# Kernel tuning notes

Measured on AMD Instinct MI355X. Metric: run time of the kernel, lower is better.

## Reference

```python
import jax, jax.numpy as jnp
import numpy as np

D_MODEL = 2048
N_HEADS = 16
HEAD_DIM = D_MODEL // N_HEADS
ROPE_THETA = 10000.0
B, S = 2, 2048
MAX_POS = 8192


def _rope(x, position_ids):
    # x: [b, h, s, hd]; position_ids: [b, s] int
    half = HEAD_DIM // 2
    inv_freq = 1.0 / (ROPE_THETA ** (jnp.arange(0, HEAD_DIM, 2, dtype=jnp.float32) / HEAD_DIM))  # [half]
    ang = position_ids[..., None].astype(jnp.float32) * inv_freq  # [b, s, half]
    cos = jnp.concatenate([jnp.cos(ang), jnp.cos(ang)], axis=-1)[:, None]  # [b, 1, s, hd]
    sin = jnp.concatenate([jnp.sin(ang), jnp.sin(ang)], axis=-1)[:, None]
    x1, x2 = x[..., :half], x[..., half:]
    rot = jnp.concatenate([-x2, x1], axis=-1)  # rotate_half
    return x * cos + rot * sin


def setup_inputs() -> dict:
    key = jax.random.key(0)
    ks = jax.random.split(key, 6)
    wscale = 1.0 / np.sqrt(D_MODEL)
    x_sparse = jax.random.normal(ks[0], (B, S, D_MODEL), dtype=jnp.float32)
    Wq = jax.random.normal(ks[1], (D_MODEL, D_MODEL), dtype=jnp.float32) * wscale
    Wk = jax.random.normal(ks[2], (D_MODEL, D_MODEL), dtype=jnp.float32) * wscale
    Wv = jax.random.normal(ks[3], (D_MODEL, D_MODEL), dtype=jnp.float32) * wscale
    Wo = jax.random.normal(ks[4], (D_MODEL, D_MODEL), dtype=jnp.float32) * wscale
    position_ids = jnp.sort(jax.random.randint(ks[5], (B, S), 0, MAX_POS), axis=-1).astype(jnp.int64)
    return {"x_sparse": x_sparse, "Wq": Wq, "Wk": Wk, "Wv": Wv, "Wo": Wo, "position_ids": position_ids}


def reference(x_sparse, Wq, Wk, Wv, Wo, position_ids):
    b, s, d = x_sparse.shape

    def heads(W):
        return (x_sparse @ W).reshape(b, s, N_HEADS, HEAD_DIM).transpose(0, 2, 1, 3)  # [b,h,s,hd]

    q = _rope(heads(Wq), position_ids)
    k = _rope(heads(Wk), position_ids)
    v = heads(Wv)

    scores = jnp.einsum('bhqd,bhkd->bhqk', q, k) / np.float32(np.sqrt(HEAD_DIM))
    # dynamic position-based causal mask: pos_i >= pos_j, broadcast over heads
    mask = position_ids[:, None, :, None] >= position_ids[:, None, None, :]  # [b,1,s,s]
    scores = jnp.where(mask, scores, jnp.float32(-1e30))
    attn = jax.nn.softmax(scores, axis=-1)
    out = jnp.einsum('bhqk,bhkd->bhqd', attn, v)  # [b,h,s,hd]
    out = out.transpose(0, 2, 1, 3).reshape(b, s, d)
    return out @ Wo
```

## Files before the change

kernel.cpp:

```cpp
#include <hip/hip_runtime.h>
#include <stdint.h>


typedef unsigned short u16;
typedef unsigned int u32;
typedef __attribute__((ext_vector_type(8))) short bf16x8;
typedef __attribute__((ext_vector_type(4))) float f32x4;

#define SEQ 2048
#define DM 2048
#define NH 16
#define HD 128
#define SM_SCALE 0.08838834764831845f
#define K2LOG 0.12751743f

__device__ __forceinline__ u16 f2bf(float f) {
  union { float f; uint32_t u; } v; v.f = f;
  uint32_t u = v.u + 0x7fffu + ((v.u >> 16) & 1u);
  return (u16)(u >> 16);
}
__device__ __forceinline__ float bf2f(u16 h) {
  union { uint32_t u; float f; } v; v.u = ((uint32_t)h) << 16; return v.f;
}
__device__ __forceinline__ u32 pack2(float a, float b) {
  return (u32)f2bf(a) | ((u32)f2bf(b) << 16);
}
__device__ __forceinline__ u32 pack2_trunc(float a, float b) {
  union { float f; u32 u; } x, y; x.f = a; y.f = b;
  return (x.u >> 16) | (y.u & 0xFFFF0000u);
}

__device__ __forceinline__ void gl2lds16(const void* g, void* l) {
  __builtin_amdgcn_global_load_lds(
      (const __attribute__((address_space(1))) uint32_t*)g,
      (__attribute__((address_space(3))) uint32_t*)l, 16, 0, 0);
}

__global__ __launch_bounds__(256) void cvt_x(const float* __restrict__ x, u16* __restrict__ xb) {
  int i = blockIdx.x * 256 + threadIdx.x;
  float4 v = ((const float4*)x)[i];
  uint2 r;
  r.x = pack2(v.x, v.y);
  r.y = pack2(v.z, v.w);
  ((uint2*)xb)[i] = r;
}

__global__ __launch_bounds__(256) void wtrans(const float* __restrict__ w0, const float* __restrict__ w1,
                                              const float* __restrict__ w2, const float* __restrict__ w3,
                                              u16* __restrict__ dst) {
  const float* W = blockIdx.z == 0 ? w0 : blockIdx.z == 1 ? w1 : blockIdx.z == 2 ? w2 : w3;
  u16* D = dst + (size_t)blockIdx.z * DM * DM;
  int k0 = blockIdx.x * 32, n0 = blockIdx.y * 32;
  __shared__ u16 t[32][33];
  int tx = threadIdx.x, ty = threadIdx.y;
#pragma unroll
  for (int i = 0; i < 32; i += 8)
    t[ty + i][tx] = f2bf(W[(size_t)(k0 + ty + i) * DM + n0 + tx]);
  __syncthreads();
#pragma unroll
  for (int i = 0; i < 32; i += 8)
    D[(size_t)(n0 + ty + i) * DM + k0 + tx] = t[tx][ty + i];
}

__device__ __forceinline__ void gemm_core(const u16* __restrict__ A, const u16* __restrict__ Bt,
                                          int m0, int n0, u16* As, u16* Bs, f32x4 acc[4][4]) {
  int tid = threadIdx.x, lane = tid & 63;
  int l15 = lane & 15, quad = lane >> 4;
  int wave = tid >> 6;
  int wm = (wave >> 1) * 64, wn = (wave & 1) * 64;
  for (int k0 = 0; k0 < DM; k0 += 64) {
#pragma unroll
    for (int i = 0; i < 4; ++i) {
      int s = i * 256 + tid;
      int row = s >> 3, c = (s & 7) ^ (row & 7);
      gl2lds16(&A[(size_t)(m0 + row) * DM + k0 + c * 8], &As[(s & ~63) * 8]);
      gl2lds16(&Bt[(size_t)(n0 + row) * DM + k0 + c * 8], &Bs[(s & ~63) * 8]);
    }
    __syncthreads();
#pragma unroll
    for (int kk = 0; kk < 2; ++kk) {
      bf16x8 af[4], bfr[4];
#pragma unroll
      for (int mt = 0; mt < 4; ++mt) {
        int row = wm + mt * 16 + l15;
        int c = (kk * 4 + quad) ^ (row & 7);
        af[mt] = *(const bf16x8*)&As[row * 64 + c * 8];
      }
#pragma unroll
      for (int nt = 0; nt < 4; ++nt) {
        int row = wn + nt * 16 + l15;
        int c = (kk * 4 + quad) ^ (row & 7);
        bfr[nt] = *(const bf16x8*)&Bs[row * 64 + c * 8];
      }
#pragma unroll
      for (int mt = 0; mt < 4; ++mt)
#pragma unroll
        for (int nt = 0; nt < 4; ++nt)
          acc[mt][nt] = __builtin_amdgcn_mfma_f32_16x16x32_bf16(af[mt], bfr[nt], acc[mt][nt], 0, 0, 0);
    }
    __syncthreads();
  }
}

__global__ __launch_bounds__(256) void qkv_gemm(const u16* __restrict__ X, const u16* __restrict__ Wt,
                                                u16* __restrict__ Qo, u16* __restrict__ Ko,
                                                u16* __restrict__ Vto) {
  __shared__ u16 As[128 * 64];
  __shared__ u16 Bs[128 * 64];
  const u16* Bt = Wt + (size_t)blockIdx.z * DM * DM;
  int n0 = blockIdx.x * 128, m0 = blockIdx.y * 128;
  f32x4 acc[4][4] = {};
  gemm_core(X, Bt, m0, n0, As, Bs, acc);
  int lane = threadIdx.x & 63, wave = threadIdx.x >> 6;
  int l15 = lane & 15, quad = lane >> 4;
  int wm = (wave >> 1) * 64, wn = (wave & 1) * 64;
  if (blockIdx.z == 2) {
    int h = n0 >> 7;
#pragma unroll
    for (int mt = 0; mt < 4; ++mt)
#pragma unroll
      for (int nt = 0; nt < 4; ++nt) {
        int tok = m0 + wm + mt * 16 + quad * 4;
        int d = wn + nt * 16 + l15;
        int b = tok >> 11, sx = tok & (SEQ - 1);
        u16* dp = &Vto[((size_t)(b * NH + h) * HD + d) * SEQ + sx];
        *(u32*)&dp[0] = pack2(acc[mt][nt][0], acc[mt][nt][1]);
        *(u32*)&dp[2] = pack2(acc[mt][nt][2], acc[mt][nt][3]);
      }
  } else {
    u16* C = blockIdx.z == 0 ? Qo : Ko;
#pragma unroll
    for (int mt = 0; mt < 4; ++mt)
#pragma unroll
      for (int nt = 0; nt < 4; ++nt)
#pragma unroll
        for (int r = 0; r < 4; ++r)
          C[(size_t)(m0 + wm + mt * 16 + quad * 4 + r) * DM + n0 + wn + nt * 16 + l15]
              = f2bf(acc[mt][nt][r]);
  }
}

__global__ __launch_bounds__(256) void proj_gemm(const u16* __restrict__ A, const u16* __restrict__ Wt,
                                                 float* __restrict__ C) {
  __shared__ u16 As[128 * 64];
  __shared__ u16 Bs[128 * 64];
  int n0 = blockIdx.x * 128, m0 = blockIdx.y * 128;
  f32x4 acc[4][4] = {};
  gemm_core(A, Wt, m0, n0, As, Bs, acc);
  int lane = threadIdx.x & 63, wave = threadIdx.x >> 6;
  int l15 = lane & 15, quad = lane >> 4;
  int wm = (wave >> 1) * 64, wn = (wave & 1) * 64;
#pragma unroll
  for (int mt = 0; mt < 4; ++mt)
#pragma unroll
    for (int nt = 0; nt < 4; ++nt)
#pragma unroll
      for (int r = 0; r < 4; ++r)
        C[(size_t)(m0 + wm + mt * 16 + quad * 4 + r) * DM + n0 + wn + nt * 16 + l15] = acc[mt][nt][r];
}

__global__ __launch_bounds__(256) void rope_k(u16* __restrict__ Q, u16* __restrict__ K,
                                              const int* __restrict__ pos) {
  uint32_t idx = blockIdx.x * 256 + threadIdx.x;
  int i = idx & 63;
  int h = (idx >> 6) & 15;
  int s = (idx >> 10) & 2047;
  int b = idx >> 21;
  u16* P = (blockIdx.y == 0) ? Q : K;
  int p = pos[b * SEQ + s];
  float inv_rev = exp2f(fmaf((float)i, -0.20762051f, -2.6514961f));
  float pf = (float)p;
  float hi = pf * inv_rev;
  float err = fmaf(pf, inv_rev, -hi);
  float r = (hi - truncf(hi)) + err;
  float ang = r * 6.2831853f;
  float sn = __sinf(ang), cs = __cosf(ang);
  size_t base = ((size_t)(b * SEQ + s)) * DM + h * HD;
  float x1 = bf2f(P[base + i]), x2 = bf2f(P[base + 64 + i]);
  P[base + i] = f2bf(x1 * cs - x2 * sn);
  P[base + 64 + i] = f2bf(x2 * cs + x1 * sn);
}

__global__ __launch_bounds__(256, 2) void attn_k(const u16* __restrict__ Q, const u16* __restrict__ K,
                                                 const u16* __restrict__ Vt, const int* __restrict__ pos,
                                                 u16* __restrict__ AO) {
  int tid = threadIdx.x, lane = tid & 63, wave = tid >> 6;
  int J = blockIdx.x * 4 + wave;
  int bh = J & 31;
  int t = J >> 5;
  int stripe = (t < 32) ? (2 * t) : (127 - 2 * t);
  int b = bh >> 4, h = bh & 15;
  int l15 = lane & 15, quad = lane >> 4;
  const int* posb = pos + b * SEQ;
  int qbase = stripe * 32;
  const u16* Kbase = &K[(size_t)(b * SEQ) * DM + h * HD];
  const u16* Vbase = &Vt[(size_t)(b * NH + h) * HD * SEQ];

  bf16x8 qf[2][4];
#pragma unroll
  for (int qi = 0; qi < 2; ++qi)
#pragma unroll
    for (int kk = 0; kk < 4; ++kk)
      qf[qi][kk] = *(const bf16x8*)&Q[(size_t)(b * SEQ + qbase + qi * 16 + l15) * DM
                                      + h * HD + kk * 32 + quad * 8];

  auto ub = [&](int v) {
    int c = 0;
#pragma unroll
    for (int st = 1024; st; st >>= 1)
      if (posb[c + st - 1] <= v) c += st;
    if (c == 2047 && posb[2047] <= v) c = 2048;
    return c;
  };
  int cnt[2];
  cnt[0] = ub(posb[qbase + l15]);
  cnt[1] = ub(posb[qbase + 16 + l15]);
  int cnt_min = ub(posb[qbase]);
  int cnt_max = ub(posb[qbase + 31]);
  int ntile = (cnt_max + 63) >> 6;

  float m_i[2] = {-1.0e30f, -1.0e30f}, l_i[2] = {0.0f, 0.0f};
  f32x4 oacc[2][8] = {};

  int base0 = l15 + ((quad & 1) << 5);
  bool hi_sel = (quad >> 1) != 0;

  for (int j = 0; j < ntile; ++j) {
    int j0 = j * 64;
    bf16x8 kf[4][4];
#pragma unroll
    for (int kk = 0; kk < 4; ++kk)
#pragma unroll
      for (int kt = 0; kt < 4; ++kt)
        kf[kk][kt] = *(const bf16x8*)&Kbase[(size_t)(j0 + kt * 16 + l15) * DM + kk * 32 + quad * 8];

    f32x4 sacc[2][4] = {};
#pragma unroll
    for (int kk = 0; kk < 4; ++kk)
#pragma unroll
      for (int qi = 0; qi < 2; ++qi)
#pragma unroll
        for (int kt = 0; kt < 4; ++kt)
          sacc[qi][kt] = __builtin_amdgcn_mfma_f32_16x16x32_bf16(kf[kk][kt], qf[qi][kk], sacc[qi][kt], 0, 0, 0);

    bf16x8 vf[2][8];
#pragma unroll
    for (int kk2 = 0; kk2 < 2; ++kk2)
#pragma unroll
      for (int dt = 0; dt < 8; ++dt)
        vf[kk2][dt] = *(const bf16x8*)&Vbase[(size_t)(dt * 16 + l15) * SEQ + j0 + kk2 * 32 + quad * 8];

    bool need_mask = (j0 + 64 > cnt_min);
    u32 pb[2][4][2];
#pragma unroll
    for (int qi = 0; qi < 2; ++qi) {
      if (need_mask) {
        int rel = cnt[qi] - j0;
#pragma unroll
        for (int kt = 0; kt < 4; ++kt)
#pragma unroll
          for (int r = 0; r < 4; ++r)
            if (kt * 16 + quad * 4 + r >= rel) sacc[qi][kt][r] = -1.0e30f;
      }
      float mx = fmaxf(fmaxf(sacc[qi][0][0], sacc[qi][0][1]), fmaxf(sacc[qi][0][2], sacc[qi][0][3]));
#pragma unroll
      for (int kt = 1; kt < 4; ++kt)
        mx = fmaxf(mx, fmaxf(fmaxf(sacc[qi][kt][0], sacc[qi][kt][1]),
                             fmaxf(sacc[qi][kt][2], sacc[qi][kt][3])));
      mx = fmaxf(mx, __shfl_xor(mx, 16));
      mx = fmaxf(mx, __shfl_xor(mx, 32));
      float mold = m_i[qi];
      float mn = fmaxf(mold, mx);
      if (__any(mn > mold)) {
        float al = exp2f((mold - mn) * K2LOG);
        l_i[qi] *= al;
#pragma unroll
        for (int dt = 0; dt < 8; ++dt) oacc[qi][dt] *= al;
        m_i[qi] = mn;
      }
      float nc = -m_i[qi] * K2LOG;
      float rs = 0.0f;
#pragma unroll
      for (int kt = 0; kt < 4; ++kt) {
        float p0 = exp2f(fmaf(sacc[qi][kt][0], K2LOG, nc));
        float p1 = exp2f(fmaf(sacc[qi][kt][1], K2LOG, nc));
        float p2 = exp2f(fmaf(sacc[qi][kt][2], K2LOG, nc));
        float p3 = exp2f(fmaf(sacc[qi][kt][3], K2LOG, nc));
        rs += (p0 + p1) + (p2 + p3);
        pb[qi][kt][0] = pack2_trunc(p0, p1);
        pb[qi][kt][1] = pack2_trunc(p2, p3);
      }
      rs += __shfl_xor(rs, 16);
      rs += __shfl_xor(rs, 32);
      l_i[qi] += rs;
    }

#pragma unroll
    for (int kk2 = 0; kk2 < 2; ++kk2) {
#pragma unroll
      for (int qi = 0; qi < 2; ++qi) {
        u32 w[4];
#pragma unroll
        for (int wd = 0; wd < 4; ++wd) {
          int src = base0 + ((wd >> 1) << 4);
          u32 va = __shfl(pb[qi][kk2 * 2 + 0][wd & 1], src);
          u32 vb = __shfl(pb[qi][kk2 * 2 + 1][wd & 1], src);
          w[wd] = hi_sel ? vb : va;
        }
        union { bf16x8 v; u32 u[4]; } pt;
        pt.u[0] = w[0]; pt.u[1] = w[1]; pt.u[2] = w[2]; pt.u[3] = w[3];
#pragma unroll
        for (int dt = 0; dt < 8; ++dt)
          oacc[qi][dt] = __builtin_amdgcn_mfma_f32_16x16x32_bf16(vf[kk2][dt], pt.v, oacc[qi][dt], 0, 0, 0);
      }
    }
  }

#pragma unroll
  for (int qi = 0; qi < 2; ++qi) {
    float inv = 1.0f / l_i[qi];
    u16* aop = &AO[(size_t)(b * SEQ + qbase + qi * 16 + l15) * DM + h * HD];
#pragma unroll
    for (int dt = 0; dt < 8; ++dt) {
      int col = dt * 16 + quad * 4;
      *(u32*)&aop[col]     = pack2(oacc[qi][dt][0] * inv, oacc[qi][dt][1] * inv);
      *(u32*)&aop[col + 2] = pack2(oacc[qi][dt][2] * inv, oacc[qi][dt][3] * inv);
    }
  }
}

extern "C" void kernel_launch(void* const* d_in, const int* in_sizes, int n_in,
                              void* d_out, int out_size, void* d_ws, size_t ws_size,
                              hipStream_t stream) {
  const float* x  = (const float*)d_in[0];
  const float* Wq = (const float*)d_in[1];
  const float* Wk = (const float*)d_in[2];
  const float* Wv = (const float*)d_in[3];
  const float* Wo = (const float*)d_in[4];
  const int*  pos = (const int*)d_in[5];
  float* out = (float*)d_out;

  u16* ws  = (u16*)d_ws;
  u16* xb  = ws;
  u16* wt  = xb  + (size_t)4096 * 2048;
  u16* qb  = wt  + (size_t)4 * 2048 * 2048;
  u16* kb  = qb  + (size_t)4096 * 2048;
  u16* vtb = kb  + (size_t)4096 * 2048;
  u16* aob = vtb + (size_t)4096 * 2048;

  cvt_x<<<8192, 256, 0, stream>>>(x, xb);
  wtrans<<<dim3(64, 64, 4), dim3(32, 8), 0, stream>>>(Wq, Wk, Wv, Wo, wt);
  qkv_gemm<<<dim3(16, 32, 3), 256, 0, stream>>>(xb, wt, qb, kb, vtb);
  rope_k<<<dim3(16384, 2), 256, 0, stream>>>(qb, kb, pos);
  attn_k<<<dim3(512), 256, 0, stream>>>(qb, kb, vtb, pos, aob);
  proj_gemm<<<dim3(16, 32), 256, 0, stream>>>(aob, wt + (size_t)3 * 2048 * 2048, out);
}
```

Before: 451.5 us.

## Split attention KV tiles across wave pairs and merge partial softmax via LDS

Each 32-row query stripe is now handled by two waves that process alternating 64-key tiles, and their partial max, sum and output accumulators are combined through shared memory at the end. The grid doubles and launch bounds rise to four blocks per CU. The aim is more parallelism and better latency hiding on the long causal stripes of the attention kernel. The cost is about 36KB of LDS per block, a block-wide barrier plus a merge step, and added register pressure from the higher occupancy target, which may cause spills.

Result: slower. 848.4 us (+87.9%).

```diff
diff --git a/kernel.cpp b/kernel.cpp
--- a/kernel.cpp
+++ b/kernel.cpp
@@ -181,11 +181,16 @@
   P[base + 64 + i] = f2bf(x2 * cs + x1 * sn);
 }
 
-__global__ __launch_bounds__(256, 2) void attn_k(const u16* __restrict__ Q, const u16* __restrict__ K,
+__global__ __launch_bounds__(256, 4) void attn_k(const u16* __restrict__ Q, const u16* __restrict__ K,
                                                  const u16* __restrict__ Vt, const int* __restrict__ pos,
                                                  u16* __restrict__ AO) {
+  __shared__ f32x4 ldsO[2][2][8][64];
+  __shared__ float ldsM[2][2][64];
+  __shared__ float ldsL[2][2][64];
   int tid = threadIdx.x, lane = tid & 63, wave = tid >> 6;
-  int J = blockIdx.x * 4 + wave;
+  int pair = wave >> 1;
+  int half = wave & 1;
+  int J = blockIdx.x * 2 + pair;
   int bh = J & 31;
   int t = J >> 5;
   int stripe = (t < 32) ? (2 * t) : (127 - 2 * t);
@@ -225,7 +230,7 @@
   int base0 = l15 + ((quad & 1) << 5);
   bool hi_sel = (quad >> 1) != 0;
 
-  for (int j = 0; j < ntile; ++j) {
+  for (int j = half; j < ntile; j += 2) {
     int j0 = j * 64;
     bf16x8 kf[4][4];
 #pragma unroll
@@ -316,15 +321,35 @@
     }
   }
 
-#pragma unroll
-  for (int qi = 0; qi < 2; ++qi) {
-    float inv = 1.0f / l_i[qi];
-    u16* aop = &AO[(size_t)(b * SEQ + qbase + qi * 16 + l15) * DM + h * HD];
-#pragma unroll
-    for (int dt = 0; dt < 8; ++dt) {
-      int col = dt * 16 + quad * 4;
-      *(u32*)&aop[col]     = pack2(oacc[qi][dt][0] * inv, oacc[qi][dt][1] * inv);
-      *(u32*)&aop[col + 2] = pack2(oacc[qi][dt][2] * inv, oacc[qi][dt][3] * inv);
+  if (half) {
+#pragma unroll
+    for (int qi = 0; qi < 2; ++qi) {
+      ldsM[pair][qi][lane] = m_i[qi];
+      ldsL[pair][qi][lane] = l_i[qi];
+#pragma unroll
+      for (int dt = 0; dt < 8; ++dt) ldsO[pair][qi][dt][lane] = oacc[qi][dt];
+    }
+  }
+  __syncthreads();
+  if (!half) {
+#pragma unroll
+    for (int qi = 0; qi < 2; ++qi) {
+      float mB = ldsM[pair][qi][lane];
+      float lB = ldsL[pair][qi][lane];
+      float mN = fmaxf(m_i[qi], mB);
+      float aA = exp2f((m_i[qi] - mN) * K2LOG);
+      float aB = exp2f((mB - mN) * K2LOG);
+      float inv = 1.0f / fmaf(l_i[qi], aA, lB * aB);
+      float sA = aA * inv, sB = aB * inv;
+      u16* aop = &AO[(size_t)(b * SEQ + qbase + qi * 16 + l15) * DM + h * HD];
+#pragma unroll
+      for (int dt = 0; dt < 8; ++dt) {
+        f32x4 ob = ldsO[pair][qi][dt][lane];
+        f32x4 oa = oacc[qi][dt];
+        int col = dt * 16 + quad * 4;
+        *(u32*)&aop[col]     = pack2(fmaf(oa[0], sA, ob[0] * sB), fmaf(oa[1], sA, ob[1] * sB));
+        *(u32*)&aop[col + 2] = pack2(fmaf(oa[2], sA, ob[2] * sB), fmaf(oa[3], sA, ob[3] * sB));
+      }
     }
   }
 }
@@ -352,6 +377,6 @@
   wtrans<<<dim3(64, 64, 4), dim3(32, 8), 0, stream>>>(Wq, Wk, Wv, Wo, wt);
   qkv_gemm<<<dim3(16, 32, 3), 256, 0, stream>>>(xb, wt, qb, kb, vtb);
   rope_k<<<dim3(16384, 2), 256, 0, stream>>>(qb, kb, pos);
-  attn_k<<<dim3(512), 256, 0, stream>>>(qb, kb, vtb, pos, aob);
+  attn_k<<<dim3(1024), 256, 0, stream>>>(qb, kb, vtb, pos, aob);
   proj_gemm<<<dim3(16, 32), 256, 0, stream>>>(aob, wt + (size_t)3 * 2048 * 2048, out);
 }
```

## Shrink attention per-wave query tile to 16 rows for higher occupancy

Applied to the files above, without the earlier changes.

Each wave in the attention kernel now handles 16 query rows instead of 32, and the grid doubles to 1024 blocks. Launch bounds rise to 4 blocks per CU, and K/V fragments are loaded per inner step rather than all at once, which cuts register pressure. The aim is more resident waves to hide global-load latency. In exchange, each K/V tile loaded from global memory is reused across half as many query rows, so total K/V traffic roughly doubles.

Result: slower. 576.1 us (+27.6%).

```diff
diff --git a/kernel.cpp b/kernel.cpp
--- a/kernel.cpp
+++ b/kernel.cpp
@@ -181,28 +181,26 @@
   P[base + 64 + i] = f2bf(x2 * cs + x1 * sn);
 }
 
-__global__ __launch_bounds__(256, 2) void attn_k(const u16* __restrict__ Q, const u16* __restrict__ K,
+__global__ __launch_bounds__(256, 4) void attn_k(const u16* __restrict__ Q, const u16* __restrict__ K,
                                                  const u16* __restrict__ Vt, const int* __restrict__ pos,
                                                  u16* __restrict__ AO) {
   int tid = threadIdx.x, lane = tid & 63, wave = tid >> 6;
   int J = blockIdx.x * 4 + wave;
   int bh = J & 31;
   int t = J >> 5;
-  int stripe = (t < 32) ? (2 * t) : (127 - 2 * t);
+  int stripe = (t < 64) ? (2 * t) : (255 - 2 * t);
   int b = bh >> 4, h = bh & 15;
   int l15 = lane & 15, quad = lane >> 4;
   const int* posb = pos + b * SEQ;
-  int qbase = stripe * 32;
+  int qbase = stripe * 16;
   const u16* Kbase = &K[(size_t)(b * SEQ) * DM + h * HD];
   const u16* Vbase = &Vt[(size_t)(b * NH + h) * HD * SEQ];
 
-  bf16x8 qf[2][4];
-#pragma unroll
-  for (int qi = 0; qi < 2; ++qi)
-#pragma unroll
-    for (int kk = 0; kk < 4; ++kk)
-      qf[qi][kk] = *(const bf16x8*)&Q[(size_t)(b * SEQ + qbase + qi * 16 + l15) * DM
-                                      + h * HD + kk * 32 + quad * 8];
+  bf16x8 qf[4];
+#pragma unroll
+  for (int kk = 0; kk < 4; ++kk)
+    qf[kk] = *(const bf16x8*)&Q[(size_t)(b * SEQ + qbase + l15) * DM
+                                + h * HD + kk * 32 + quad * 8];
 
   auto ub = [&](int v) {
     int c = 0;
@@ -212,120 +210,105 @@
     if (c == 2047 && posb[2047] <= v) c = 2048;
     return c;
   };
-  int cnt[2];
-  cnt[0] = ub(posb[qbase + l15]);
-  cnt[1] = ub(posb[qbase + 16 + l15]);
+  int cnt = ub(posb[qbase + l15]);
   int cnt_min = ub(posb[qbase]);
-  int cnt_max = ub(posb[qbase + 31]);
+  int cnt_max = ub(posb[qbase + 15]);
   int ntile = (cnt_max + 63) >> 6;
 
-  float m_i[2] = {-1.0e30f, -1.0e30f}, l_i[2] = {0.0f, 0.0f};
-  f32x4 oacc[2][8] = {};
+  float m_i = -1.0e30f, l_i = 0.0f;
+  f32x4 oacc[8] = {};
 
   int base0 = l15 + ((quad & 1) << 5);
   bool hi_sel = (quad >> 1) != 0;
 
   for (int j = 0; j < ntile; ++j) {
     int j0 = j * 64;
-    bf16x8 kf[4][4];
-#pragma unroll
-    for (int kk = 0; kk < 4; ++kk)
-#pragma unroll
-      for (int kt = 0; kt < 4; ++kt)
-        kf[kk][kt] = *(const bf16x8*)&Kbase[(size_t)(j0 + kt * 16 + l15) * DM + kk * 32 + quad * 8];
-
-    f32x4 sacc[2][4] = {};
-#pragma unroll
-    for (int kk = 0; kk < 4; ++kk)
-#pragma unroll
-      for (int qi = 0; qi < 2; ++qi)
+
+    f32x4 sacc[4] = {};
+#pragma unroll
+    for (int kt = 0; kt < 4; ++kt) {
+      bf16x8 kfa[4];
+#pragma unroll
+      for (int kk = 0; kk < 4; ++kk)
+        kfa[kk] = *(const bf16x8*)&Kbase[(size_t)(j0 + kt * 16 + l15) * DM + kk * 32 + quad * 8];
+#pragma unroll
+      for (int kk = 0; kk < 4; ++kk)
+        sacc[kt] = __builtin_amdgcn_mfma_f32_16x16x32_bf16(kfa[kk], qf[kk], sacc[kt], 0, 0, 0);
+    }
+
+    bool need_mask = (j0 + 64 > cnt_min);
+    u32 pb[4][2];
+    {
+      if (need_mask) {
+        int rel = cnt - j0;
 #pragma unroll
         for (int kt = 0; kt < 4; ++kt)
-          sacc[qi][kt] = __builtin_amdgcn_mfma_f32_16x16x32_bf16(kf[kk][kt], qf[qi][kk], sacc[qi][kt], 0, 0, 0);
-
-    bf16x8 vf[2][8];
-#pragma unroll
-    for (int kk2 = 0; kk2 < 2; ++kk2)
-#pragma unroll
-      for (int dt = 0; dt < 8; ++dt)
-        vf[kk2][dt] = *(const bf16x8*)&Vbase[(size_t)(dt * 16 + l15) * SEQ + j0 + kk2 * 32 + quad * 8];
-
-    bool need_mask = (j0 + 64 > cnt_min);
-    u32 pb[2][4][2];
-#pragma unroll
-    for (int qi = 0; qi < 2; ++qi) {
-      if (need_mask) {
-        int rel = cnt[qi] - j0;
-#pragma unroll
-        for (int kt = 0; kt < 4; ++kt)
 #pragma unroll
           for (int r = 0; r < 4; ++r)
-            if (kt * 16 + quad * 4 + r >= rel) sacc[qi][kt][r] = -1.0e30f;
-      }
-      float mx = fmaxf(fmaxf(sacc[qi][0][0], sacc[qi][0][1]), fmaxf(sacc[qi][0][2], sacc[qi][0][3]));
+            if (kt * 16 + quad * 4 + r >= rel) sacc[kt][r] = -1.0e30f;
+      }
+      float mx = fmaxf(fmaxf(sacc[0][0], sacc[0][1]), fmaxf(sacc[0][2], sacc[0][3]));
 #pragma unroll
       for (int kt = 1; kt < 4; ++kt)
-        mx = fmaxf(mx, fmaxf(fmaxf(sacc[qi][kt][0], sacc[qi][kt][1]),
-                             fmaxf(sacc[qi][kt][2], sacc[qi][kt][3])));
+        mx = fmaxf(mx, fmaxf(fmaxf(sacc[kt][0], sacc[kt][1]),
+                             fmaxf(sacc[kt][2], sacc[kt][3])));
       mx = fmaxf(mx, __shfl_xor(mx, 16));
       mx = fmaxf(mx, __shfl_xor(mx, 32));
-      float mold = m_i[qi];
+      float mold = m_i;
       float mn = fmaxf(mold, mx);
       if (__any(mn > mold)) {
         float al = exp2f((mold - mn) * K2LOG);
-        l_i[qi] *= al;
-#pragma unroll
-        for (int dt = 0; dt < 8; ++dt) oacc[qi][dt] *= al;
-        m_i[qi] = mn;
-      }
-      float nc = -m_i[qi] * K2LOG;
+        l_i *= al;
+#pragma unroll
+        for (int dt = 0; dt < 8; ++dt) oacc[dt] *= al;
+        m_i = mn;
+      }
+      float nc = -m_i * K2LOG;
       float rs = 0.0f;
 #pragma unroll
       for (int kt = 0; kt < 4; ++kt) {
-        float p0 = exp2f(fmaf(sacc[qi][kt][0], K2LOG, nc));
-        float p1 = exp2f(fmaf(sacc[qi][kt][1], K2LOG, nc));
-        float p2 = exp2f(fmaf(sacc[qi][kt][2], K2LOG, nc));
-        float p3 = exp2f(fmaf(sacc[qi][kt][3], K2LOG, nc));
+        float p0 = exp2f(fmaf(sacc[kt][0], K2LOG, nc));
+        float p1 = exp2f(fmaf(sacc[kt][1], K2LOG, nc));
+        float p2 = exp2f(fmaf(sacc[kt][2], K2LOG, nc));
+        float p3 = exp2f(fmaf(sacc[kt][3], K2LOG, nc));
         rs += (p0 + p1) + (p2 + p3);
-        pb[qi][kt][0] = pack2_trunc(p0, p1);
-        pb[qi][kt][1] = pack2_trunc(p2, p3);
+        pb[kt][0] = pack2_trunc(p0, p1);
+        pb[kt][1] = pack2_trunc(p2, p3);
       }
       rs += __shfl_xor(rs, 16);
       rs += __shfl_xor(rs, 32);
-      l_i[qi] += rs;
+      l_i += rs;
     }
 
 #pragma unroll
     for (int kk2 = 0; kk2 < 2; ++kk2) {
-#pragma unroll
-      for (int qi = 0; qi < 2; ++qi) {
-        u32 w[4];
-#pragma unroll
-        for (int wd = 0; wd < 4; ++wd) {
-          int src = base0 + ((wd >> 1) << 4);
-          u32 va = __shfl(pb[qi][kk2 * 2 + 0][wd & 1], src);
-          u32 vb = __shfl(pb[qi][kk2 * 2 + 1][wd & 1], src);
-          w[wd] = hi_sel ? vb : va;
-        }
-        union { bf16x8 v; u32 u[4]; } pt;
-        pt.u[0] = w[0]; pt.u[1] = w[1]; pt.u[2] = w[2]; pt.u[3] = w[3];
-#pragma unroll
-        for (int dt = 0; dt < 8; ++dt)
-          oacc[qi][dt] = __builtin_amdgcn_mfma_f32_16x16x32_bf16(vf[kk2][dt], pt.v, oacc[qi][dt], 0, 0, 0);
-      }
+      bf16x8 vf[8];
+#pragma unroll
+      for (int dt = 0; dt < 8; ++dt)
+        vf[dt] = *(const bf16x8*)&Vbase[(size_t)(dt * 16 + l15) * SEQ + j0 + kk2 * 32 + quad * 8];
+      u32 w[4];
+#pragma unroll
+      for (int wd = 0; wd < 4; ++wd) {
+        int src = base0 + ((wd >> 1) << 4);
+        u32 va = __shfl(pb[kk2 * 2 + 0][wd & 1], src);
+        u32 vb = __shfl(pb[kk2 * 2 + 1][wd & 1], src);
+        w[wd] = hi_sel ? vb : va;
+      }
+      union { bf16x8 v; u32 u[4]; } pt;
+      pt.u[0] = w[0]; pt.u[1] = w[1]; pt.u[2] = w[2]; pt.u[3] = w[3];
+#pragma unroll
+      for (int dt = 0; dt < 8; ++dt)
+        oacc[dt] = __builtin_amdgcn_mfma_f32_16x16x32_bf16(vf[dt], pt.v, oacc[dt], 0, 0, 0);
     }
   }
 
-#pragma unroll
-  for (int qi = 0; qi < 2; ++qi) {
-    float inv = 1.0f / l_i[qi];
-    u16* aop = &AO[(size_t)(b * SEQ + qbase + qi * 16 + l15) * DM + h * HD];
-#pragma unroll
-    for (int dt = 0; dt < 8; ++dt) {
-      int col = dt * 16 + quad * 4;
-      *(u32*)&aop[col]     = pack2(oacc[qi][dt][0] * inv, oacc[qi][dt][1] * inv);
-      *(u32*)&aop[col + 2] = pack2(oacc[qi][dt][2] * inv, oacc[qi][dt][3] * inv);
-    }
+  float inv = 1.0f / l_i;
+  u16* aop = &AO[(size_t)(b * SEQ + qbase + l15) * DM + h * HD];
+#pragma unroll
+  for (int dt = 0; dt < 8; ++dt) {
+    int col = dt * 16 + quad * 4;
+    *(u32*)&aop[col]     = pack2(oacc[dt][0] * inv, oacc[dt][1] * inv);
+    *(u32*)&aop[col + 2] = pack2(oacc[dt][2] * inv, oacc[dt][3] * inv);
   }
 }
 
@@ -352,6 +335,6 @@
   wtrans<<<dim3(64, 64, 4), dim3(32, 8), 0, stream>>>(Wq, Wk, Wv, Wo, wt);
   qkv_gemm<<<dim3(16, 32, 3), 256, 0, stream>>>(xb, wt, qb, kb, vtb);
   rope_k<<<dim3(16384, 2), 256, 0, stream>>>(qb, kb, pos);
-  attn_k<<<dim3(512), 256, 0, stream>>>(qb, kb, vtb, pos, aob);
+  attn_k<<<dim3(1024), 256, 0, stream>>>(qb, kb, vtb, pos, aob);
   proj_gemm<<<dim3(16, 32), 256, 0, stream>>>(aob, wt + (size_t)3 * 2048 * 2048, out);
 }
```

## Share K/V tiles across waves via double-buffered LDS staging in attention

Applied to the files above, without the earlier changes.

Each block now handles four adjacent query stripes of the same batch-head instead of four independent stripes. K and V tiles are staged once per block into swizzled, double-buffered LDS with async global-to-LDS copies, replacing the per-wave direct global loads. The block-level tile count follows the last stripe, and waves with fewer tiles idle through the barriers. This cuts redundant global/L2 traffic at the cost of 64KB of LDS, per-tile __syncthreads, and load imbalance between waves.

Result: faster. 425.5 us (-5.8%).

```diff
diff --git a/kernel.cpp b/kernel.cpp
--- a/kernel.cpp
+++ b/kernel.cpp
@@ -184,17 +184,20 @@
 __global__ __launch_bounds__(256, 2) void attn_k(const u16* __restrict__ Q, const u16* __restrict__ K,
                                                  const u16* __restrict__ Vt, const int* __restrict__ pos,
                                                  u16* __restrict__ AO) {
+  __shared__ u16 Ks[2][64 * 128];
+  __shared__ u16 Vs[2][128 * 64];
   int tid = threadIdx.x, lane = tid & 63, wave = tid >> 6;
-  int J = blockIdx.x * 4 + wave;
-  int bh = J & 31;
-  int t = J >> 5;
-  int stripe = (t < 32) ? (2 * t) : (127 - 2 * t);
+  int bx = blockIdx.x;
+  int bh = bx & 31;
+  int g4 = bx >> 5;
+  int g = (bh & 1) ? (15 - g4) : g4;
   int b = bh >> 4, h = bh & 15;
+  int stripe = 4 * g + wave;
   int l15 = lane & 15, quad = lane >> 4;
   const int* posb = pos + b * SEQ;
   int qbase = stripe * 32;
-  const u16* Kbase = &K[(size_t)(b * SEQ) * DM + h * HD];
-  const u16* Vbase = &Vt[(size_t)(b * NH + h) * HD * SEQ];
+  const u16* Kg = &K[(size_t)(b * SEQ) * DM + h * HD];
+  const u16* Vg = &Vt[(size_t)(b * NH + h) * HD * SEQ];
 
   bf16x8 qf[2][4];
 #pragma unroll
@@ -218,6 +221,22 @@
   int cnt_min = ub(posb[qbase]);
   int cnt_max = ub(posb[qbase + 31]);
   int ntile = (cnt_max + 63) >> 6;
+  int cnt_blk = ub(posb[(4 * g + 3) * 32 + 31]);
+  int ntile_blk = (cnt_blk + 63) >> 6;
+
+  auto STAGE = [&](int j0, int bufi) {
+#pragma unroll
+    for (int i = 0; i < 4; ++i) {
+      int s = i * 256 + tid;
+      int rk = s >> 4, ck = (s & 15) ^ (rk & 15);
+      gl2lds16(&Kg[(size_t)(j0 + rk) * DM + ck * 8], &Ks[bufi][(s & ~63) * 8]);
+      int rv = s >> 3, cv = (s & 7) ^ (rv & 7);
+      gl2lds16(&Vg[(size_t)rv * SEQ + j0 + cv * 8], &Vs[bufi][(s & ~63) * 8]);
+    }
+  };
+
+  STAGE(0, 0);
+  __syncthreads();
 
   float m_i[2] = {-1.0e30f, -1.0e30f}, l_i[2] = {0.0f, 0.0f};
   f32x4 oacc[2][8] = {};
@@ -225,95 +244,101 @@
   int base0 = l15 + ((quad & 1) << 5);
   bool hi_sel = (quad >> 1) != 0;
 
-  for (int j = 0; j < ntile; ++j) {
-    int j0 = j * 64;
-    bf16x8 kf[4][4];
-#pragma unroll
-    for (int kk = 0; kk < 4; ++kk)
-#pragma unroll
-      for (int kt = 0; kt < 4; ++kt)
-        kf[kk][kt] = *(const bf16x8*)&Kbase[(size_t)(j0 + kt * 16 + l15) * DM + kk * 32 + quad * 8];
-
-    f32x4 sacc[2][4] = {};
-#pragma unroll
-    for (int kk = 0; kk < 4; ++kk)
-#pragma unroll
-      for (int qi = 0; qi < 2; ++qi)
-#pragma unroll
-        for (int kt = 0; kt < 4; ++kt)
-          sacc[qi][kt] = __builtin_amdgcn_mfma_f32_16x16x32_bf16(kf[kk][kt], qf[qi][kk], sacc[qi][kt], 0, 0, 0);
-
-    bf16x8 vf[2][8];
-#pragma unroll
-    for (int kk2 = 0; kk2 < 2; ++kk2)
-#pragma unroll
-      for (int dt = 0; dt < 8; ++dt)
-        vf[kk2][dt] = *(const bf16x8*)&Vbase[(size_t)(dt * 16 + l15) * SEQ + j0 + kk2 * 32 + quad * 8];
-
-    bool need_mask = (j0 + 64 > cnt_min);
-    u32 pb[2][4][2];
-#pragma unroll
-    for (int qi = 0; qi < 2; ++qi) {
-      if (need_mask) {
-        int rel = cnt[qi] - j0;
-#pragma unroll
-        for (int kt = 0; kt < 4; ++kt)
-#pragma unroll
-          for (int r = 0; r < 4; ++r)
-            if (kt * 16 + quad * 4 + r >= rel) sacc[qi][kt][r] = -1.0e30f;
-      }
-      float mx = fmaxf(fmaxf(sacc[qi][0][0], sacc[qi][0][1]), fmaxf(sacc[qi][0][2], sacc[qi][0][3]));
-#pragma unroll
-      for (int kt = 1; kt < 4; ++kt)
-        mx = fmaxf(mx, fmaxf(fmaxf(sacc[qi][kt][0], sacc[qi][kt][1]),
-                             fmaxf(sacc[qi][kt][2], sacc[qi][kt][3])));
-      mx = fmaxf(mx, __shfl_xor(mx, 16));
-      mx = fmaxf(mx, __shfl_xor(mx, 32));
-      float mold = m_i[qi];
-      float mn = fmaxf(mold, mx);
-      if (__any(mn > mold)) {
-        float al = exp2f((mold - mn) * K2LOG);
-        l_i[qi] *= al;
-#pragma unroll
-        for (int dt = 0; dt < 8; ++dt) oacc[qi][dt] *= al;
-        m_i[qi] = mn;
-      }
-      float nc = -m_i[qi] * K2LOG;
-      float rs = 0.0f;
+  for (int j = 0; j < ntile_blk; ++j) {
+    int cur = j & 1;
+    if (j + 1 < ntile_blk) STAGE((j + 1) * 64, cur ^ 1);
+
+    if (j < ntile) {
+      int j0 = j * 64;
+
+      f32x4 sacc[2][4] = {};
 #pragma unroll
       for (int kt = 0; kt < 4; ++kt) {
-        float p0 = exp2f(fmaf(sacc[qi][kt][0], K2LOG, nc));
-        float p1 = exp2f(fmaf(sacc[qi][kt][1], K2LOG, nc));
-        float p2 = exp2f(fmaf(sacc[qi][kt][2], K2LOG, nc));
-        float p3 = exp2f(fmaf(sacc[qi][kt][3], K2LOG, nc));
-        rs += (p0 + p1) + (p2 + p3);
-        pb[qi][kt][0] = pack2_trunc(p0, p1);
-        pb[qi][kt][1] = pack2_trunc(p2, p3);
-      }
-      rs += __shfl_xor(rs, 16);
-      rs += __shfl_xor(rs, 32);
-      l_i[qi] += rs;
-    }
-
-#pragma unroll
-    for (int kk2 = 0; kk2 < 2; ++kk2) {
+        bf16x8 kfa[4];
+#pragma unroll
+        for (int kk = 0; kk < 4; ++kk) {
+          int cs = (kk * 4 + quad) ^ l15;
+          kfa[kk] = *(const bf16x8*)&Ks[cur][((kt * 16 + l15) * 16 + cs) * 8];
+        }
+#pragma unroll
+        for (int qi = 0; qi < 2; ++qi)
+#pragma unroll
+          for (int kk = 0; kk < 4; ++kk)
+            sacc[qi][kt] = __builtin_amdgcn_mfma_f32_16x16x32_bf16(kfa[kk], qf[qi][kk], sacc[qi][kt], 0, 0, 0);
+      }
+
+      bool need_mask = (j0 + 64 > cnt_min);
+      u32 pb[2][4][2];
 #pragma unroll
       for (int qi = 0; qi < 2; ++qi) {
-        u32 w[4];
-#pragma unroll
-        for (int wd = 0; wd < 4; ++wd) {
-          int src = base0 + ((wd >> 1) << 4);
-          u32 va = __shfl(pb[qi][kk2 * 2 + 0][wd & 1], src);
-          u32 vb = __shfl(pb[qi][kk2 * 2 + 1][wd & 1], src);
-          w[wd] = hi_sel ? vb : va;
-        }
-        union { bf16x8 v; u32 u[4]; } pt;
-        pt.u[0] = w[0]; pt.u[1] = w[1]; pt.u[2] = w[2]; pt.u[3] = w[3];
-#pragma unroll
-        for (int dt = 0; dt < 8; ++dt)
-          oacc[qi][dt] = __builtin_amdgcn_mfma_f32_16x16x32_bf16(vf[kk2][dt], pt.v, oacc[qi][dt], 0, 0, 0);
-      }
-    }
+        if (need_mask) {
+          int rel = cnt[qi] - j0;
+#pragma unroll
+          for (int kt = 0; kt < 4; ++kt)
+#pragma unroll
+            for (int r = 0; r < 4; ++r)
+              if (kt * 16 + quad * 4 + r >= rel) sacc[qi][kt][r] = -1.0e30f;
+        }
+        float mx = fmaxf(fmaxf(sacc[qi][0][0], sacc[qi][0][1]), fmaxf(sacc[qi][0][2], sacc[qi][0][3]));
+#pragma unroll
+        for (int kt = 1; kt < 4; ++kt)
+          mx = fmaxf(mx, fmaxf(fmaxf(sacc[qi][kt][0], sacc[qi][kt][1]),
+                               fmaxf(sacc[qi][kt][2], sacc[qi][kt][3])));
+        mx = fmaxf(mx, __shfl_xor(mx, 16));
+        mx = fmaxf(mx, __shfl_xor(mx, 32));
+        float mold = m_i[qi];
+        float mn = fmaxf(mold, mx);
+        if (__any(mn > mold)) {
+          float al = exp2f((mold - mn) * K2LOG);
+          l_i[qi] *= al;
+#pragma unroll
+          for (int dt = 0; dt < 8; ++dt) oacc[qi][dt] *= al;
+          m_i[qi] = mn;
+        }
+        float nc = -m_i[qi] * K2LOG;
+        float rs = 0.0f;
+#pragma unroll
+        for (int kt = 0; kt < 4; ++kt) {
+          float p0 = exp2f(fmaf(sacc[qi][kt][0], K2LOG, nc));
+          float p1 = exp2f(fmaf(sacc[qi][kt][1], K2LOG, nc));
+          float p2 = exp2f(fmaf(sacc[qi][kt][2], K2LOG, nc));
+          float p3 = exp2f(fmaf(sacc[qi][kt][3], K2LOG, nc));
+          rs += (p0 + p1) + (p2 + p3);
+          pb[qi][kt][0] = pack2_trunc(p0, p1);
+          pb[qi][kt][1] = pack2_trunc(p2, p3);
+        }
+        rs += __shfl_xor(rs, 16);
+        rs += __shfl_xor(rs, 32);
+        l_i[qi] += rs;
+      }
+
+#pragma unroll
+      for (int kk2 = 0; kk2 < 2; ++kk2) {
+        bf16x8 vf[8];
+#pragma unroll
+        for (int dt = 0; dt < 8; ++dt) {
+          int cs = (kk2 * 4 + quad) ^ (l15 & 7);
+          vf[dt] = *(const bf16x8*)&Vs[cur][((dt * 16 + l15) * 8 + cs) * 8];
+        }
+#pragma unroll
+        for (int qi = 0; qi < 2; ++qi) {
+          u32 w[4];
+#pragma unroll
+          for (int wd = 0; wd < 4; ++wd) {
+            int src = base0 + ((wd >> 1) << 4);
+            u32 va = __shfl(pb[qi][kk2 * 2 + 0][wd & 1], src);
+            u32 vb = __shfl(pb[qi][kk2 * 2 + 1][wd & 1], src);
+            w[wd] = hi_sel ? vb : va;
+          }
+          union { bf16x8 v; u32 u[4]; } pt;
+          pt.u[0] = w[0]; pt.u[1] = w[1]; pt.u[2] = w[2]; pt.u[3] = w[3];
+#pragma unroll
+          for (int dt = 0; dt < 8; ++dt)
+            oacc[qi][dt] = __builtin_amdgcn_mfma_f32_16x16x32_bf16(vf[dt], pt.v, oacc[qi][dt], 0, 0, 0);
+        }
+      }
+    }
+    __syncthreads();
   }
 
 #pragma unroll
```
